# Performance work log

Hardware: AMD Instinct MI355X
Metric: run time of the kernel (lower is better)

The kernel has to match this reference:

```python
import jax, jax.numpy as jnp
import numpy as np

DIM = 128
POS_HID = 64
ATTN_HID = DIM * 4
K_NEIGH = 16


def _mlp2(x, w1, b1, w2, b2):
    # Linear -> ReLU -> Linear (weights stored as (in, out))
    return jax.nn.relu(x @ w1 + b1) @ w2 + b2


def setup_inputs() -> dict:
    key = jax.random.key(0)
    ks = jax.random.split(key, 12)
    B, N = 2, 512
    s = 0.05
    return {
        "x": jax.random.normal(ks[0], (B, DIM, N), jnp.float32),
        "pos": jax.random.normal(ks[1], (B, N, 3), jnp.float32),
        "w_qkv": jax.random.normal(ks[2], (DIM, 3 * DIM), jnp.float32) * s,
        "pos_w1": jax.random.normal(ks[3], (3, POS_HID), jnp.float32) * s,
        "pos_b1": jnp.zeros((POS_HID,), jnp.float32),
        "pos_w2": jax.random.normal(ks[4], (POS_HID, DIM), jnp.float32) * s,
        "pos_b2": jnp.zeros((DIM,), jnp.float32),
        "attn_w1": jax.random.normal(ks[5], (DIM, ATTN_HID), jnp.float32) * s,
        "attn_b1": jnp.zeros((ATTN_HID,), jnp.float32),
        "attn_w2": jax.random.normal(ks[6], (ATTN_HID, DIM), jnp.float32) * s,
        "attn_b2": jnp.zeros((DIM,), jnp.float32),
    }


def reference(x, pos, w_qkv, pos_w1, pos_b1, pos_w2, pos_b2,
              attn_w1, attn_b1, attn_w2, attn_b2):
    # x: (B, dim, N) -> (B, N, dim)
    xt = jnp.swapaxes(x, 1, 2)
    B, N, d = xt.shape

    qkv = xt @ w_qkv                           # (B, N, 3d), no bias
    q, k, v = jnp.split(qkv, 3, axis=-1)

    rel_pos = pos[:, :, None, :] - pos[:, None, :, :]          # (B, N, N, 3)
    rel_pos_emb = _mlp2(rel_pos, pos_w1, pos_b1, pos_w2, pos_b2)  # (B, N, N, d)
    qk_rel = q[:, :, None, :] - k[:, None, :, :]               # (B, N, N, d)

    # KNN: smallest euclidean rel distances per query point
    rel_dist = jnp.sqrt(jnp.sum(rel_pos * rel_pos, axis=-1))   # (B, N, N)
    _, idx = jax.lax.top_k(-rel_dist, K_NEIGH)                 # (B, N, K)

    idxe = idx[..., None]                                      # (B, N, K, 1)
    v_g = v[jnp.arange(B)[:, None, None], idx]                 # (B, N, K, d)
    qk_g = jnp.take_along_axis(qk_rel, idxe, axis=2)           # (B, N, K, d)
    pe_g = jnp.take_along_axis(rel_pos_emb, idxe, axis=2)      # (B, N, K, d)

    v_g = v_g + pe_g
    sim = _mlp2(qk_g + pe_g, attn_w1, attn_b1, attn_w2, attn_b2)  # (B, N, K, d)
    attn = jax.nn.softmax(sim, axis=-2)                        # softmax over neighbors
    agg = jnp.einsum('bikd,bikd->bid', attn, v_g)              # (B, N, d)
    return jnp.swapaxes(agg, 1, 2)                             # (B, d, N)
```

## Files before the change

### kernel.cpp

```cpp
#include <hip/hip_runtime.h>
#include <math.h>

#define DIM 128
#define N_PTS 512
#define K_NEIGH 16
#define POS_HID 64
#define ATTN_HID 512

typedef __attribute__((ext_vector_type(8))) short short8;
typedef __attribute__((ext_vector_type(4))) float f32x4;
typedef unsigned short us;
typedef unsigned long long ull;

__device__ __forceinline__ us f2b(float f) {
    unsigned int u = __builtin_bit_cast(unsigned int, f);
    u += 0x7fffu + ((u >> 16) & 1u);
    return (us)(u >> 16);
}

__device__ __forceinline__ ull shflx64(ull v, int m) {
    int lo = __shfl_xor((int)(unsigned int)v, m);
    int hi = __shfl_xor((int)(unsigned int)(v >> 32), m);
    return ((ull)(unsigned int)hi << 32) | (unsigned int)lo;
}

__global__ void pack_kernel(const float* __restrict__ wqkv,
                            const float* __restrict__ aw1,
                            const float* __restrict__ aw2,
                            const float* __restrict__ pw2,
                            us* __restrict__ p0, us* __restrict__ p1,
                            us* __restrict__ p2, us* __restrict__ p3) {
    int t = blockIdx.x * 256 + threadIdx.x;
    if (t < 49152) {
        int j = t & 7, l = (t >> 3) & 63, rem = t >> 9;
        int nt = rem % 24, ks = rem / 24;
        int k = ks * 32 + (l >> 4) * 8 + j, n = nt * 16 + (l & 15);
        p0[t] = f2b(wqkv[k * 384 + n]);
    } else if (t < 114688) {
        int u = t - 49152;
        int j = u & 7, l = (u >> 3) & 63, nt = (u >> 9) & 31, ks = u >> 14;
        int k = ks * 32 + (l >> 4) * 8 + j, n = nt * 16 + (l & 15);
        p1[u] = f2b(aw1[k * ATTN_HID + n]);
    } else if (t < 180224) {
        int u = t - 114688;
        int j = u & 7, l = (u >> 3) & 63, nt = (u >> 9) & 7, ch = u >> 12;
        int k = ch * 32 + (l >> 4) * 8 + j, n = nt * 16 + (l & 15);
        p2[u] = f2b(aw2[k * DIM + n]);
    } else if (t < 188416) {
        int u = t - 180224;
        int j = u & 7, l = (u >> 3) & 63, nt = (u >> 9) & 7, ks = u >> 12;
        int k = ks * 32 + (l >> 4) * 8 + j, n = nt * 16 + (l & 15);
        p3[u] = f2b(pw2[k * DIM + n]);
    }
}

__global__ __launch_bounds__(512)
void qkv_mfma_kernel(const float* __restrict__ x,
                     const us* __restrict__ p0,
                     float* __restrict__ qkv) {
    __shared__ __align__(16) us xA[16][136];
    const int tid = threadIdx.x;
    const int w = tid >> 6, lane = tid & 63, quad = lane >> 4, lq = lane & 15;
    const int n0 = blockIdx.x * 16;
    const int b = n0 >> 9, nn = n0 & (N_PTS - 1);
#pragma unroll
    for (int rr = 0; rr < 4; ++rr) {
        int id = rr * 512 + tid;
        int d = id >> 4, i = id & 15;
        xA[i][d] = f2b(x[(size_t)(b * DIM + d) * N_PTS + nn + i]);
    }
    __syncthreads();
    short8 a[4];
#pragma unroll
    for (int ks = 0; ks < 4; ++ks)
        a[ks] = *(const short8*)&xA[lq][ks * 32 + quad * 8];
#pragma unroll
    for (int i = 0; i < 3; ++i) {
        int nt = w * 3 + i;
        f32x4 acc = {0.f, 0.f, 0.f, 0.f};
#pragma unroll
        for (int ks = 0; ks < 4; ++ks) {
            const short8 bf = *(const short8*)(p0 + (size_t)((ks * 24 + nt) * 64 + lane) * 8);
            acc = __builtin_amdgcn_mfma_f32_16x16x32_bf16(a[ks], bf, acc, 0, 0, 0);
        }
#pragma unroll
        for (int r = 0; r < 4; ++r)
            qkv[(size_t)(n0 + quad * 4 + r) * 384 + nt * 16 + lq] = acc[r];
    }
}

__global__ __launch_bounds__(256, 1)
void attn_fused_kernel(const float* __restrict__ pos,
                       const float* __restrict__ qkv,
                       const float* __restrict__ pw1,
                       const float* __restrict__ pb1,
                       const float* __restrict__ pb2,
                       const us* __restrict__ p1,
                       const us* __restrict__ p2,
                       const us* __restrict__ p3,
                       const float* __restrict__ ab1,
                       float* __restrict__ out) {
    __shared__ __align__(16) us hinA[4][16][136];
    __shared__ __align__(16) us h1s[4][16][40];
    __shared__ int nbrs[4][16];

    const int tid = threadIdx.x;
    const int w = tid >> 6, lane = tid & 63, quad = lane >> 4, lq = lane & 15;
    const int g = blockIdx.x * 4 + w, b = g >> 9, n = g & (N_PTS - 1);

    short8 b3f[2][8];
#pragma unroll
    for (int ks = 0; ks < 2; ++ks)
#pragma unroll
        for (int nt = 0; nt < 8; ++nt)
            b3f[ks][nt] = *(const short8*)(p3 + (size_t)((ks * 8 + nt) * 64 + lane) * 8);

    float w1x[2][8], w1y[2][8], w1z[2][8], w1b[2][8];
#pragma unroll
    for (int ks = 0; ks < 2; ++ks)
#pragma unroll
        for (int jj = 0; jj < 8; ++jj) {
            int c = ks * 32 + quad * 8 + jj;
            w1x[ks][jj] = pw1[c];
            w1y[ks][jj] = pw1[64 + c];
            w1z[ks][jj] = pw1[128 + c];
            w1b[ks][jj] = pb1[c];
        }

    float qvr[8], pb2r[8], ab1r[32];
#pragma unroll
    for (int nt = 0; nt < 8; ++nt) {
        qvr[nt]  = qkv[(size_t)g * 384 + nt * 16 + lq];
        pb2r[nt] = pb2[nt * 16 + lq];
    }
#pragma unroll
    for (int nt = 0; nt < 32; ++nt) ab1r[nt] = ab1[nt * 16 + lq];

    {
        const float pix = pos[g * 3 + 0], piy = pos[g * 3 + 1], piz = pos[g * 3 + 2];
        float d2[8];
#pragma unroll
        for (int rr = 0; rr < 8; ++rr) {
            int j = rr * 64 + lane;
            float dx = pix - pos[(b * N_PTS + j) * 3 + 0];
            float dy = piy - pos[(b * N_PTS + j) * 3 + 1];
            float dz = piz - pos[(b * N_PTS + j) * 3 + 2];
            d2[rr] = dx * dx + dy * dy + dz * dz;
        }
        for (int r = 0; r < K_NEIGH; ++r) {
            ull key = ~0ULL;
#pragma unroll
            for (int rr = 0; rr < 8; ++rr) {
                unsigned int fb = __builtin_bit_cast(unsigned int, d2[rr]);
                ull k2 = ((ull)fb << 32) | (unsigned int)(rr * 64 + lane);
                key = k2 < key ? k2 : key;
            }
#pragma unroll
            for (int off = 32; off > 0; off >>= 1) {
                ull o = shflx64(key, off);
                key = o < key ? o : key;
            }
            unsigned int jw = (unsigned int)key;
            if (lane == 0) nbrs[w][r] = (int)jw;
            if (lane == (int)(jw & 63)) d2[jw >> 6] = __builtin_inff();
        }
    }

    short8 pha[2];
    {
        const int jn = nbrs[w][lq];
        float rx = pos[g * 3 + 0] - pos[(b * N_PTS + jn) * 3 + 0];
        float ry = pos[g * 3 + 1] - pos[(b * N_PTS + jn) * 3 + 1];
        float rz = pos[g * 3 + 2] - pos[(b * N_PTS + jn) * 3 + 2];
#pragma unroll
        for (int ks = 0; ks < 2; ++ks) {
            short8 f;
#pragma unroll
            for (int jj = 0; jj < 8; ++jj) {
                float h = rx * w1x[ks][jj] + ry * w1y[ks][jj] + rz * w1z[ks][jj] + w1b[ks][jj];
                f[jj] = (short)f2b(fmaxf(h, 0.f));
            }
            pha[ks] = f;
        }
    }

    f32x4 pe[8];
#pragma unroll
    for (int nt = 0; nt < 8; ++nt) {
        f32x4 acc = {0.f, 0.f, 0.f, 0.f};
        acc = __builtin_amdgcn_mfma_f32_16x16x32_bf16(pha[0], b3f[0][nt], acc, 0, 0, 0);
        acc = __builtin_amdgcn_mfma_f32_16x16x32_bf16(pha[1], b3f[1][nt], acc, 0, 0, 0);
#pragma unroll
        for (int r = 0; r < 4; ++r) pe[nt][r] = acc[r] + pb2r[nt];
    }

    f32x4 vg[8];
    {
        int jr[4];
#pragma unroll
        for (int r = 0; r < 4; ++r) jr[r] = nbrs[w][quad * 4 + r];
#pragma unroll
        for (int nt = 0; nt < 8; ++nt) {
            int d = nt * 16 + lq;
#pragma unroll
            for (int r = 0; r < 4; ++r) {
                const float* kv = qkv + (size_t)(b * N_PTS + jr[r]) * 384;
                float pp = pe[nt][r];
                hinA[w][quad * 4 + r][d] = f2b(qvr[nt] - kv[128 + d] + pp);
                vg[nt][r] = kv[256 + d] + pp;
            }
        }
    }

    short8 a1f[4];
#pragma unroll
    for (int ks = 0; ks < 4; ++ks)
        a1f[ks] = *(const short8*)&hinA[w][lq][ks * 32 + quad * 8];

    f32x4 c2[8];
#pragma unroll
    for (int nt = 0; nt < 8; ++nt) c2[nt] = (f32x4){0.f, 0.f, 0.f, 0.f};

    short8 p1f[2][2][4];
    short8 p2f[2][8];
#pragma unroll
    for (int t = 0; t < 2; ++t)
#pragma unroll
        for (int ks = 0; ks < 4; ++ks)
            p1f[0][t][ks] = *(const short8*)(p1 + (size_t)(((ks << 5) + t) * 64 + lane) * 8);
#pragma unroll
    for (int nt2 = 0; nt2 < 8; ++nt2)
        p2f[0][nt2] = *(const short8*)(p2 + (size_t)(nt2 * 64 + lane) * 8);

#pragma unroll
    for (int ch = 0; ch < 16; ++ch) {
        const int cur = ch & 1, nxt = cur ^ 1;
        if (ch < 15) {
#pragma unroll
            for (int t = 0; t < 2; ++t)
#pragma unroll
                for (int ks = 0; ks < 4; ++ks)
                    p1f[nxt][t][ks] = *(const short8*)(p1 + (size_t)(((ks << 5) + (ch + 1) * 2 + t) * 64 + lane) * 8);
        }
#pragma unroll
        for (int t = 0; t < 2; ++t) {
            int nt = ch * 2 + t;
            f32x4 acc = {0.f, 0.f, 0.f, 0.f};
#pragma unroll
            for (int ks = 0; ks < 4; ++ks)
                acc = __builtin_amdgcn_mfma_f32_16x16x32_bf16(a1f[ks], p1f[cur][t][ks], acc, 0, 0, 0);
            float bias = ab1r[nt];
#pragma unroll
            for (int r = 0; r < 4; ++r)
                h1s[w][quad * 4 + r][t * 16 + lq] = f2b(fmaxf(acc[r] + bias, 0.f));
        }
        if (ch < 15) {
#pragma unroll
            for (int nt2 = 0; nt2 < 8; ++nt2)
                p2f[nxt][nt2] = *(const short8*)(p2 + (size_t)((((ch + 1) << 3) + nt2) * 64 + lane) * 8);
        }
        const short8 a2 = *(const short8*)&h1s[w][lq][quad * 8];
#pragma unroll
        for (int nt2 = 0; nt2 < 8; ++nt2)
            c2[nt2] = __builtin_amdgcn_mfma_f32_16x16x32_bf16(a2, p2f[cur][nt2], c2[nt2], 0, 0, 0);
    }

#pragma unroll
    for (int nt2 = 0; nt2 < 8; ++nt2) {
        f32x4 s4 = c2[nt2];
        float m = fmaxf(fmaxf(s4[0], s4[1]), fmaxf(s4[2], s4[3]));
        m = fmaxf(m, __shfl_xor(m, 16));
        m = fmaxf(m, __shfl_xor(m, 32));
        float e0 = __expf(s4[0] - m), e1 = __expf(s4[1] - m);
        float e2 = __expf(s4[2] - m), e3 = __expf(s4[3] - m);
        float s = e0 + e1 + e2 + e3;
        f32x4 v4 = vg[nt2];
        float a = e0 * v4[0] + e1 * v4[1] + e2 * v4[2] + e3 * v4[3];
        s += __shfl_xor(s, 16); s += __shfl_xor(s, 32);
        a += __shfl_xor(a, 16); a += __shfl_xor(a, 32);
        if (quad == 0)
            out[(size_t)(b * DIM + nt2 * 16 + lq) * N_PTS + n] = a / s;
    }
}

extern "C" void kernel_launch(void* const* d_in, const int* in_sizes, int n_in,
                              void* d_out, int out_size, void* d_ws, size_t ws_size,
                              hipStream_t stream) {
    const float* x    = (const float*)d_in[0];
    const float* pos  = (const float*)d_in[1];
    const float* wqkv = (const float*)d_in[2];
    const float* pw1  = (const float*)d_in[3];
    const float* pb1  = (const float*)d_in[4];
    const float* pw2  = (const float*)d_in[5];
    const float* pb2  = (const float*)d_in[6];
    const float* aw1  = (const float*)d_in[7];
    const float* ab1  = (const float*)d_in[8];
    const float* aw2  = (const float*)d_in[9];
    float* out = (float*)d_out;

    int B = in_sizes[0] / (DIM * N_PTS);
    int npts = B * N_PTS;

    char* ws = (char*)d_ws;
    float* qkv = (float*)ws;
    us* p0 = (us*)(ws + (size_t)npts * 384 * 4);
    us* p1 = p0 + 49152;
    us* p2 = p1 + 65536;
    us* p3 = p2 + 65536;

    pack_kernel<<<736, 256, 0, stream>>>(wqkv, aw1, aw2, pw2, p0, p1, p2, p3);
    qkv_mfma_kernel<<<npts / 16, 512, 0, stream>>>(x, p0, qkv);
    attn_fused_kernel<<<npts / 4, 256, 0, stream>>>(pos, qkv,
                                                    pw1, pb1, pb2,
                                                    p1, p2, p3, ab1, out);
}
```

Before: 100.00 us.

## Stage attention MLP weights in shared LDS double buffer across warps

Before, each of the four warps separately streamed the attention MLP weight fragments (p1, p2) from global memory into registers. Now the whole block loads each chunk cooperatively into a double-buffered LDS area, and every warp reads its MFMA B operands from LDS. This cuts global/L2 traffic per block by four and frees registers. The cost is a __syncthreads per chunk, about 32KB of extra LDS, and LDS read latency on the MFMA critical path.

```diff
diff --git a/kernel.cpp b/kernel.cpp
--- a/kernel.cpp
+++ b/kernel.cpp
@@ -102,11 +102,34 @@
                        float* __restrict__ out) {
     __shared__ __align__(16) us hinA[4][16][136];
     __shared__ __align__(16) us h1s[4][16][40];
+    __shared__ __align__(16) us wbuf[2][8192];
     __shared__ int nbrs[4][16];
 
     const int tid = threadIdx.x;
     const int w = tid >> 6, lane = tid & 63, quad = lane >> 4, lq = lane & 15;
     const int g = blockIdx.x * 4 + w, b = g >> 9, n = g & (N_PTS - 1);
+
+    {
+        short8 s0[4];
+        if (tid < 128) {
+            const int piece = tid >> 5, sub = tid & 31;
+            const us* src = p1 + (size_t)((piece << 5) * 512) + sub * 8;
+#pragma unroll
+            for (int i = 0; i < 4; ++i) s0[i] = *(const short8*)(src + i * 256);
+            us* d = &wbuf[0][piece * 1024 + sub * 8];
+#pragma unroll
+            for (int i = 0; i < 4; ++i) *(short8*)(d + i * 256) = s0[i];
+        } else {
+            const int u = tid - 128;
+            const us* src = p2 + (size_t)(u * 8);
+#pragma unroll
+            for (int i = 0; i < 4; ++i) s0[i] = *(const short8*)(src + i * 1024);
+            us* d = &wbuf[0][4096 + u * 8];
+#pragma unroll
+            for (int i = 0; i < 4; ++i) *(short8*)(d + i * 1024) = s0[i];
+        }
+    }
+    __syncthreads();
 
     short8 b3f[2][8];
 #pragma unroll
@@ -221,48 +244,57 @@
 #pragma unroll
     for (int nt = 0; nt < 8; ++nt) c2[nt] = (f32x4){0.f, 0.f, 0.f, 0.f};
 
-    short8 p1f[2][2][4];
-    short8 p2f[2][8];
-#pragma unroll
-    for (int t = 0; t < 2; ++t)
-#pragma unroll
-        for (int ks = 0; ks < 4; ++ks)
-            p1f[0][t][ks] = *(const short8*)(p1 + (size_t)(((ks << 5) + t) * 64 + lane) * 8);
-#pragma unroll
-    for (int nt2 = 0; nt2 < 8; ++nt2)
-        p2f[0][nt2] = *(const short8*)(p2 + (size_t)(nt2 * 64 + lane) * 8);
-
 #pragma unroll
     for (int ch = 0; ch < 16; ++ch) {
         const int cur = ch & 1, nxt = cur ^ 1;
+        short8 stmp[4];
         if (ch < 15) {
-#pragma unroll
-            for (int t = 0; t < 2; ++t)
-#pragma unroll
-                for (int ks = 0; ks < 4; ++ks)
-                    p1f[nxt][t][ks] = *(const short8*)(p1 + (size_t)(((ks << 5) + (ch + 1) * 2 + t) * 64 + lane) * 8);
+            if (tid < 128) {
+                const int piece = tid >> 5, sub = tid & 31;
+                const us* src = p1 + (size_t)((((piece << 5) + (ch + 1) * 2)) * 512) + sub * 8;
+#pragma unroll
+                for (int i = 0; i < 4; ++i) stmp[i] = *(const short8*)(src + i * 256);
+            } else {
+                const int u = tid - 128;
+                const us* src = p2 + (size_t)(((ch + 1) << 3) * 512) + u * 8;
+#pragma unroll
+                for (int i = 0; i < 4; ++i) stmp[i] = *(const short8*)(src + i * 1024);
+            }
         }
 #pragma unroll
         for (int t = 0; t < 2; ++t) {
             int nt = ch * 2 + t;
             f32x4 acc = {0.f, 0.f, 0.f, 0.f};
 #pragma unroll
-            for (int ks = 0; ks < 4; ++ks)
-                acc = __builtin_amdgcn_mfma_f32_16x16x32_bf16(a1f[ks], p1f[cur][t][ks], acc, 0, 0, 0);
+            for (int ks = 0; ks < 4; ++ks) {
+                const short8 bf = *(const short8*)&wbuf[cur][(ks * 2 + t) * 512 + lane * 8];
+                acc = __builtin_amdgcn_mfma_f32_16x16x32_bf16(a1f[ks], bf, acc, 0, 0, 0);
+            }
             float bias = ab1r[nt];
 #pragma unroll
             for (int r = 0; r < 4; ++r)
                 h1s[w][quad * 4 + r][t * 16 + lq] = f2b(fmaxf(acc[r] + bias, 0.f));
         }
+        const short8 a2 = *(const short8*)&h1s[w][lq][quad * 8];
+#pragma unroll
+        for (int nt2 = 0; nt2 < 8; ++nt2) {
+            const short8 bf2 = *(const short8*)&wbuf[cur][(8 + nt2) * 512 + lane * 8];
+            c2[nt2] = __builtin_amdgcn_mfma_f32_16x16x32_bf16(a2, bf2, c2[nt2], 0, 0, 0);
+        }
         if (ch < 15) {
-#pragma unroll
-            for (int nt2 = 0; nt2 < 8; ++nt2)
-                p2f[nxt][nt2] = *(const short8*)(p2 + (size_t)((((ch + 1) << 3) + nt2) * 64 + lane) * 8);
-        }
-        const short8 a2 = *(const short8*)&h1s[w][lq][quad * 8];
-#pragma unroll
-        for (int nt2 = 0; nt2 < 8; ++nt2)
-            c2[nt2] = __builtin_amdgcn_mfma_f32_16x16x32_bf16(a2, p2f[cur][nt2], c2[nt2], 0, 0, 0);
+            if (tid < 128) {
+                const int piece = tid >> 5, sub = tid & 31;
+                us* d = &wbuf[nxt][piece * 1024 + sub * 8];
+#pragma unroll
+                for (int i = 0; i < 4; ++i) *(short8*)(d + i * 256) = stmp[i];
+            } else {
+                const int u = tid - 128;
+                us* d = &wbuf[nxt][4096 + u * 8];
+#pragma unroll
+                for (int i = 0; i < 4; ++i) *(short8*)(d + i * 1024) = stmp[i];
+            }
+        }
+        __syncthreads();
     }
 
 #pragma unroll
```

After: 105.7 us. 1.06x slower.
